# Kernel tuning notes

Hardware: AMD Instinct MI355X
Metric: run time of the kernel (lower is better)

The kernel has to match this reference:

```python
import jax, jax.numpy as jnp
import numpy as np

N_HEADS = 16
KEY_DIM = 64
VAL_DIM = 64
HIDDEN = 1024
SCALE = 1.0 / float(KEY_DIM) ** 0.5


def setup_inputs() -> dict:
    key = jax.random.key(0)
    ks = jax.random.split(key, 16)
    B, Lq, Lk, R = 2, 2048, 2048, 2048
    inp = {
        "query": jax.random.normal(ks[0], (B, Lq, HIDDEN), jnp.float32),
        "value": jax.random.normal(ks[1], (B, Lk, HIDDEN), jnp.float32),
        "positional_embedding": jax.random.normal(ks[2], (R, HIDDEN), jnp.float32),
        "u_weight": jax.random.normal(ks[3], (N_HEADS, KEY_DIM), jnp.float32) * 0.02,
        "v_weight": jax.random.normal(ks[4], (N_HEADS, KEY_DIM), jnp.float32) * 0.02,
        "indices": jax.random.randint(ks[5], (2, Lq, Lk), 0, R, jnp.int64 if jax.config.jax_enable_x64 else jnp.int32),
        "lower": jax.random.uniform(ks[6], (Lq, Lk), jnp.float32),
    }
    s = 0.02
    inp["Wq"] = jax.random.normal(ks[7], (HIDDEN, N_HEADS * KEY_DIM), jnp.float32) * s
    inp["bq"] = jnp.zeros((N_HEADS * KEY_DIM,), jnp.float32)
    inp["Wk"] = jax.random.normal(ks[8], (HIDDEN, N_HEADS * KEY_DIM), jnp.float32) * s
    inp["bk"] = jnp.zeros((N_HEADS * KEY_DIM,), jnp.float32)
    inp["Wv"] = jax.random.normal(ks[9], (HIDDEN, N_HEADS * VAL_DIM), jnp.float32) * s
    inp["bv"] = jnp.zeros((N_HEADS * VAL_DIM,), jnp.float32)
    inp["Wr"] = jax.random.normal(ks[10], (HIDDEN, N_HEADS * KEY_DIM), jnp.float32) * s
    inp["br"] = jnp.zeros((N_HEADS * KEY_DIM,), jnp.float32)
    inp["Wo"] = jax.random.normal(ks[11], (N_HEADS * VAL_DIM, HIDDEN), jnp.float32) * s
    inp["bo"] = jnp.zeros((HIDDEN,), jnp.float32)
    return inp


def reference(query, value, positional_embedding, u_weight, v_weight, indices, lower,
              Wq, bq, Wk, bk, Wv, bv, Wr, br, Wo, bo):
    B, Lq, _ = query.shape
    Lk = value.shape[1]
    R = positional_embedding.shape[0]
    # projections (torch Linear with weights stored as [in, out])
    q = (query @ Wq + bq).reshape(B, Lq, N_HEADS, KEY_DIM)
    k = (value @ Wk + bk).reshape(B, Lk, N_HEADS, KEY_DIM)
    v = (value @ Wv + bv).reshape(B, Lk, N_HEADS, VAL_DIM)
    r = (positional_embedding @ Wr + br).reshape(R, N_HEADS, KEY_DIM)
    # content (AC) and position (BD) score terms -> [i, j, b, n]
    AC = jnp.einsum("bind,bjnd->ijbn", q + u_weight, k)
    BD = jnp.einsum("bind,jnd->ijbn", q + v_weight, r)
    # rel-shift: gather [Lq, R] -> [Lq, Lk] positions, then apply lower mask
    BD = BD[indices[0], indices[1]] * lower[:, :, None, None]
    attn = jax.nn.softmax((AC + BD) * SCALE, axis=1)  # softmax over key dim j
    out = jnp.einsum("ijbn,bjnd->bind", attn, v).reshape(B, Lq, N_HEADS * VAL_DIM)
    return out @ Wo + bo
```

## Files before the change

kernel.cpp:

```cpp
#include <hip/hip_runtime.h>
#include <stdint.h>

typedef __attribute__((ext_vector_type(8))) short short8;
typedef __attribute__((ext_vector_type(4))) float f32x4;
typedef unsigned short u16;
typedef unsigned int u32;

#define LQ 2048
#define LK 2048
#define RDIM 2048
#define HID 1024
#define NH 16
#define DH 64
#define XL_SCALE 0.125f

__device__ __forceinline__ float bf2f(u16 u){
  union { unsigned int i; float f; } v; v.i = ((unsigned int)u) << 16; return v.f;
}
__device__ __forceinline__ u16 f2bf(float f){
  union { float f; unsigned int i; } v; v.f = f;
  unsigned int r = v.i + 0x7fffu + ((v.i >> 16) & 1u);
  return (u16)(r >> 16);
}
__device__ __forceinline__ f32x4 fzero(){ f32x4 z = {0.0f, 0.0f, 0.0f, 0.0f}; return z; }

__global__ void k_detect(const u32* __restrict__ q, const u32* __restrict__ idxw,
                         int* __restrict__ flags){
  int t = threadIdx.x;
  u32 w = q[t];
  int b = (w >> 7) & 0xFF;
  unsigned long long mb = __ballot(b >= 100 && b <= 140);
  u32 hi = idxw[2 * t + 1];
  unsigned long long mi = __ballot(hi == 0u);
  if (t == 0){
    flags[0] = (__popcll(mb) >= 48) ? 1 : 0;
    flags[1] = (__popcll(mi) == 64) ? 1 : 0;
  }
}

struct Seg { const void* src; u16* dst; int n4; };
struct SegPack { Seg s[8]; };
__global__ void k_ingestN(SegPack p, const int* __restrict__ flags){
  int f = flags[0];
  Seg sg = p.s[blockIdx.y];
  int stride = gridDim.x * blockDim.x;
  for (int i = blockIdx.x * blockDim.x + threadIdx.x; i < sg.n4; i += stride){
    if (f){
      reinterpret_cast<uint2*>(sg.dst)[i] = reinterpret_cast<const uint2*>(sg.src)[i];
    } else {
      float4 v = reinterpret_cast<const float4*>(sg.src)[i];
      union { u16 h[4]; uint2 u; } t;
      t.h[0] = f2bf(v.x); t.h[1] = f2bf(v.y); t.h[2] = f2bf(v.z); t.h[3] = f2bf(v.w);
      reinterpret_cast<uint2*>(sg.dst)[i] = t.u;
    }
  }
}

struct WPack { const void* src[5]; u16* dst[5]; };
__global__ void k_wtrans(WPack p, const int* __restrict__ flags){
  int f = flags[0];
  const void* W = p.src[blockIdx.z];
  u16* Wt = p.dst[blockIdx.z];
  __shared__ u16 t[64][65];
  int tid = threadIdx.x;
  int bx = blockIdx.x, by = blockIdx.y;
#pragma unroll
  for (int it = 0; it < 16; ++it){
    int id = it * 256 + tid;
    int r = id >> 6, c = id & 63;
    size_t so = (size_t)(by * 64 + r) * HID + bx * 64 + c;
    t[r][c] = f ? ((const u16*)W)[so] : f2bf(((const float*)W)[so]);
  }
  __syncthreads();
#pragma unroll
  for (int it = 0; it < 16; ++it){
    int id = it * 256 + tid;
    int r = id >> 6, c = id & 63;
    Wt[(size_t)(bx * 64 + r) * HID + by * 64 + c] = t[c][r];
  }
}

__global__ void k_goff(const int* __restrict__ idx, int* __restrict__ goff,
                       const int* __restrict__ flags){
  int i64f = flags[1];
  const size_t N = (size_t)LQ * LK;
  size_t stride = (size_t)gridDim.x * blockDim.x;
  for (size_t t = (size_t)blockIdx.x * blockDim.x + threadIdx.x; t < N; t += stride){
    long long a0, a1;
    if (i64f){
      const long long* ip = (const long long*)idx;
      a0 = ip[t]; a1 = ip[N + t];
    } else {
      a0 = idx[t]; a1 = idx[N + t];
    }
    goff[t] = (int)(a0 * RDIM + a1);
  }
}

__global__ void k_gemm(const u16* __restrict__ A, const u16* __restrict__ Bt,
                       const u16* __restrict__ bias,
                       const u16* __restrict__ add0, const u16* __restrict__ add1,
                       void* __restrict__ D0, u16* __restrict__ D1,
                       int headmajor, const int* __restrict__ oflags){
  __shared__ u16 As[128][72];
  __shared__ u16 Bs[128][72];
  int tid = threadIdx.x;
  int l = tid & 63, w = tid >> 6;
  int lr = l & 15, g = l >> 4;
  int wr = w >> 1, wc = w & 1;
  int outf32 = oflags ? (oflags[0] == 0) : 0;
  f32x4 acc[4][4];
#pragma unroll
  for (int a = 0; a < 4; ++a)
#pragma unroll
    for (int bq_ = 0; bq_ < 4; ++bq_) acc[a][bq_] = fzero();
  const size_t arowg = (size_t)blockIdx.x * 128;
  const size_t browg = (size_t)blockIdx.y * 128;
  for (int kt = 0; kt < HID; kt += 64){
#pragma unroll
    for (int it = 0; it < 4; ++it){
      int id = it * 256 + tid;
      int r = id >> 3, ch = id & 7;
      uint4 va = *reinterpret_cast<const uint4*>(A + (arowg + r) * HID + kt + ch * 8);
      *reinterpret_cast<uint4*>(&As[r][ch * 8]) = va;
      uint4 vb = *reinterpret_cast<const uint4*>(Bt + (browg + r) * HID + kt + ch * 8);
      *reinterpret_cast<uint4*>(&Bs[r][ch * 8]) = vb;
    }
    __syncthreads();
#pragma unroll
    for (int ks = 0; ks < 2; ++ks){
      short8 af[4], bfv[4];
#pragma unroll
      for (int mf = 0; mf < 4; ++mf)
        af[mf] = *reinterpret_cast<const short8*>(&As[wr * 64 + mf * 16 + lr][ks * 32 + 8 * g]);
#pragma unroll
      for (int nf = 0; nf < 4; ++nf)
        bfv[nf] = *reinterpret_cast<const short8*>(&Bs[wc * 64 + nf * 16 + lr][ks * 32 + 8 * g]);
#pragma unroll
      for (int mf = 0; mf < 4; ++mf)
#pragma unroll
        for (int nf = 0; nf < 4; ++nf)
          acc[mf][nf] = __builtin_amdgcn_mfma_f32_16x16x32_bf16(af[mf], bfv[nf], acc[mf][nf], 0, 0, 0);
    }
    __syncthreads();
  }
#pragma unroll
  for (int mf = 0; mf < 4; ++mf)
#pragma unroll
    for (int nf = 0; nf < 4; ++nf){
      int col = (int)browg + wc * 64 + nf * 16 + lr;
      float bcol = bf2f(bias[col]);
      float a0 = add0 ? bf2f(add0[col]) : 0.0f;
      float a1 = add1 ? bf2f(add1[col]) : 0.0f;
#pragma unroll
      for (int reg = 0; reg < 4; ++reg){
        int row = (int)arowg + wr * 64 + mf * 16 + 4 * g + reg;
        float base = acc[mf][nf][reg] + bcol;
        size_t dst;
        if (headmajor){
          int b = row >> 11, i = row & 2047;
          int n = col >> 6, d = col & 63;
          dst = ((size_t)(b * NH + n) * LQ + i) * DH + d;
        } else {
          dst = (size_t)row * HID + col;
        }
        if (outf32) ((float*)D0)[dst] = base + a0;
        else        ((u16*)D0)[dst] = f2bf(base + a0);
        if (D1) D1[dst] = f2bf(base + a1);
      }
    }
}

template<int G>
__global__ void k_bdfull(const u16* __restrict__ qv, const u16* __restrict__ rr,
                         u16* __restrict__ bdf, int bnBase){
  __shared__ u16 tile[16][32][G];
  int tid = threadIdx.x;
  int l = tid & 63, w = tid >> 6;
  int lr = l & 15, g = l >> 4;
  int i0 = blockIdx.x * 16, j0 = blockIdx.y * 32;
  constexpr int C = (G >= 4) ? (G / 4) : 1;
  if (G >= 4 || w < G){
#pragma unroll
    for (int bi = 0; bi < C; ++bi){
      int g_ = w * C + bi;
      int bn = bnBase + g_;
      int b = bn >> 4, n = bn & 15;
      const u16* qb = qv + ((size_t)(b * NH + n) * LQ + i0) * DH;
      const u16* rb = rr + ((size_t)n * RDIM + j0) * DH;
      f32x4 acc2[2];
      acc2[0] = fzero(); acc2[1] = fzero();
#pragma unroll
      for (int ks = 0; ks < 2; ++ks){
        short8 a = *reinterpret_cast<const short8*>(qb + (size_t)lr * DH + ks * 32 + 8 * g);
#pragma unroll
        for (int nf = 0; nf < 2; ++nf){
          short8 bb = *reinterpret_cast<const short8*>(rb + (size_t)(lr + 16 * nf) * DH + ks * 32 + 8 * g);
          acc2[nf] = __builtin_amdgcn_mfma_f32_16x16x32_bf16(a, bb, acc2[nf], 0, 0, 0);
        }
      }
#pragma unroll
      for (int nf = 0; nf < 2; ++nf){
        int jj = lr + 16 * nf;
#pragma unroll
        for (int reg = 0; reg < 4; ++reg)
          tile[4 * g + reg][jj][g_] = f2bf(acc2[nf][reg]);
      }
    }
  }
  __syncthreads();
  constexpr int W = (G >= 4) ? 4 : G;
  constexpr int PARTS = G / W;
  constexpr int CHUNKS = 512 * PARTS;
#pragma unroll
  for (int e = 0; e < (CHUNKS + 255) / 256; ++e){
    int id = e * 256 + tid;
    if (CHUNKS < 256 * ((CHUNKS + 255) / 256) && id >= CHUNKS) break;
    int line = id / PARTS, part = id % PARTS;
    int ii = line >> 5, jj = line & 31;
    int k = part * W;
    const u16* src = &tile[ii][jj][k];
    u16* dst = bdf + ((size_t)(i0 + ii) * RDIM + (size_t)(j0 + jj)) * G + k;
    if (W == 4)
      *reinterpret_cast<unsigned long long*>(dst) = *reinterpret_cast<const unsigned long long*>(src);
    else if (W == 2)
      *reinterpret_cast<unsigned int*>(dst) = *reinterpret_cast<const unsigned int*>(src);
    else
      *dst = *src;
  }
}

template<int G>
__global__ void k_gather(const u16* __restrict__ bdf, const int* __restrict__ goff,
                         const u16* __restrict__ lower, u16* __restrict__ bdg){
  __shared__ u16 tile[G][16][32];
  int tid = threadIdx.x;
  int i0 = blockIdx.x * 16, j0 = blockIdx.y * 32;
#pragma unroll
  for (int it = 0; it < 2; ++it){
    int p = it * 256 + tid;
    int ii = p >> 5, jj = p & 31;
    size_t off = (size_t)(i0 + ii) * LK + (j0 + jj);
    int go = goff[off];
    float lw = bf2f(lower[off]);
    const u16* src = bdf + (size_t)go * G;
    union { uint4 q[2]; u32 w2[8]; u16 h[16]; } uv;
    if (G == 16){
      uv.q[0] = *reinterpret_cast<const uint4*>(src);
      uv.q[1] = *reinterpret_cast<const uint4*>(src + 8);
    } else if (G == 8){
      uv.q[0] = *reinterpret_cast<const uint4*>(src);
    } else if (G == 2){
      uv.w2[0] = *reinterpret_cast<const u32*>(src);
    } else {
      uv.h[0] = *src;
    }
#pragma unroll
    for (int k = 0; k < G; ++k)
      tile[k][ii][jj] = f2bf(bf2f(uv.h[k]) * lw);
  }
  __syncthreads();
  constexpr int CHUNKS = G * 128;
#pragma unroll
  for (int e = 0; e < (CHUNKS + 255) / 256; ++e){
    int id = e * 256 + tid;
    if (CHUNKS < 256 * ((CHUNKS + 255) / 256) && id >= CHUNKS) break;
    int g_ = id >> 7, rem = id & 127;
    int ii = rem >> 3, part = rem & 7;
    unsigned long long v = *reinterpret_cast<const unsigned long long*>(&tile[g_][ii][part * 4]);
    *reinterpret_cast<unsigned long long*>(
        bdg + (size_t)g_ * LQ * LK + (size_t)(i0 + ii) * LK + j0 + part * 4) = v;
  }
}

__global__ void k_flash(const u16* __restrict__ qu, const u16* __restrict__ kk,
                        const u16* __restrict__ vv, const u16* __restrict__ bdg,
                        u16* __restrict__ oo, int bnBase){
  __shared__ u16 klds[128][72];
  __shared__ u16 vtlds[64][136];
  __shared__ u16 plds[4][16][136];
  int tid = threadIdx.x;
  int l = tid & 63, w = tid >> 6;
  int lr = l & 15, g = l >> 4;
  int gi = blockIdx.x;
  int bn = bnBase + gi;
  int b = bn >> 4, n = bn & 15;
  int i0 = blockIdx.y * 64;
  const u16* qb = qu + ((size_t)bn * LQ + i0 + w * 16) * DH;
  short8 aq0 = *reinterpret_cast<const short8*>(qb + (size_t)lr * DH + 8 * g);
  short8 aq1 = *reinterpret_cast<const short8*>(qb + (size_t)lr * DH + 32 + 8 * g);
  f32x4 O[4];
#pragma unroll
  for (int nf = 0; nf < 4; ++nf) O[nf] = fzero();
  float mrun[4], lrun[4];
#pragma unroll
  for (int r = 0; r < 4; ++r){ mrun[r] = -1e30f; lrun[r] = 0.0f; }
  const u16* kbase = kk + (size_t)bn * LK * DH;
  const u16* vbase = vv + (size_t)bn * LK * DH;
  const u16* bdb = bdg + (size_t)gi * LQ * LK + (size_t)(i0 + w * 16) * LK;

  for (int j0 = 0; j0 < LK; j0 += 128){
#pragma unroll
    for (int it = 0; it < 4; ++it){
      int id = it * 256 + tid;
      int r = id >> 3, ch = id & 7;
      uint4 kv = *reinterpret_cast<const uint4*>(kbase + (size_t)(j0 + r) * DH + ch * 8);
      *reinterpret_cast<uint4*>(&klds[r][ch * 8]) = kv;
      uint4 vv4 = *reinterpret_cast<const uint4*>(vbase + (size_t)(j0 + r) * DH + ch * 8);
      u16 tmp[8];
      *reinterpret_cast<uint4*>(tmp) = vv4;
#pragma unroll
      for (int e2 = 0; e2 < 8; ++e2) vtlds[ch * 8 + e2][r] = tmp[e2];
    }
    __syncthreads();

    float sv[8][4];
#pragma unroll
    for (int nf = 0; nf < 8; ++nf){
      f32x4 z = fzero();
      short8 bk0 = *reinterpret_cast<const short8*>(&klds[lr + 16 * nf][8 * g]);
      short8 bk1 = *reinterpret_cast<const short8*>(&klds[lr + 16 * nf][32 + 8 * g]);
      z = __builtin_amdgcn_mfma_f32_16x16x32_bf16(aq0, bk0, z, 0, 0, 0);
      z = __builtin_amdgcn_mfma_f32_16x16x32_bf16(aq1, bk1, z, 0, 0, 0);
#pragma unroll
      for (int reg = 0; reg < 4; ++reg){
        float bd = bf2f(bdb[(size_t)(4 * g + reg) * LK + j0 + lr + 16 * nf]);
        sv[nf][reg] = (z[reg] + bd) * XL_SCALE;
      }
    }
    float fs[4];
#pragma unroll
    for (int reg = 0; reg < 4; ++reg){
      float mx = sv[0][reg];
#pragma unroll
      for (int nf = 1; nf < 8; ++nf) mx = fmaxf(mx, sv[nf][reg]);
#pragma unroll
      for (int d = 1; d < 16; d <<= 1) mx = fmaxf(mx, __shfl_xor(mx, d));
      float mnew = fmaxf(mrun[reg], mx);
      fs[reg] = __expf(mrun[reg] - mnew);
      mrun[reg] = mnew;
      float sum = 0.0f;
#pragma unroll
      for (int nf = 0; nf < 8; ++nf){
        sv[nf][reg] = __expf(sv[nf][reg] - mnew);
        sum += sv[nf][reg];
      }
#pragma unroll
      for (int d = 1; d < 16; d <<= 1) sum += __shfl_xor(sum, d);
      lrun[reg] = lrun[reg] * fs[reg] + sum;
    }
#pragma unroll
    for (int nf = 0; nf < 4; ++nf)
#pragma unroll
      for (int reg = 0; reg < 4; ++reg)
        O[nf][reg] *= fs[reg];
#pragma unroll
    for (int nf = 0; nf < 8; ++nf)
#pragma unroll
      for (int reg = 0; reg < 4; ++reg)
        plds[w][4 * g + reg][lr + 16 * nf] = f2bf(sv[nf][reg]);
    short8 pa[4];
#pragma unroll
    for (int ks = 0; ks < 4; ++ks)
      pa[ks] = *reinterpret_cast<const short8*>(&plds[w][lr][ks * 32 + 8 * g]);
#pragma unroll
    for (int nf = 0; nf < 4; ++nf){
#pragma unroll
      for (int ks = 0; ks < 4; ++ks){
        short8 bv = *reinterpret_cast<const short8*>(&vtlds[lr + 16 * nf][ks * 32 + 8 * g]);
        O[nf] = __builtin_amdgcn_mfma_f32_16x16x32_bf16(pa[ks], bv, O[nf], 0, 0, 0);
      }
    }
    __syncthreads();
  }
#pragma unroll
  for (int nf = 0; nf < 4; ++nf)
#pragma unroll
    for (int reg = 0; reg < 4; ++reg){
      int i = i0 + w * 16 + 4 * g + reg;
      float vo = O[nf][reg] / lrun[reg];
      oo[((size_t)(b * LQ + i)) * HID + n * DH + lr + 16 * nf] = f2bf(vo);
    }
}

extern "C" void kernel_launch(void* const* d_in, const int* in_sizes, int n_in,
                              void* d_out, int out_size, void* d_ws, size_t ws_size,
                              hipStream_t stream){
  const void* query = d_in[0];
  const void* value = d_in[1];
  const void* pos   = d_in[2];
  const void* uw    = d_in[3];
  const void* vw    = d_in[4];
  const int* idx    = (const int*)d_in[5];
  const void* lower = d_in[6];
  const void* Wq = d_in[7];  const void* bq = d_in[8];
  const void* Wk = d_in[9];  const void* bk = d_in[10];
  const void* Wv = d_in[11]; const void* bv = d_in[12];
  const void* Wr = d_in[13]; const void* br = d_in[14];
  const void* Wo = d_in[15]; const void* bo = d_in[16];
  (void)in_sizes; (void)n_in; (void)out_size;

  char* ws = (char*)d_ws;
  const size_t MB = (size_t)1 << 20;
  u16* cquery = (u16*)(ws + 0 * MB);
  u16* cvalue = (u16*)(ws + 8 * MB);
  int* goff   = (int*)(ws + 0 * MB);
  u16* cpos   = (u16*)(ws + 16 * MB);
  u16* clower = (u16*)(ws + 20 * MB);
  char* sm = ws + 38 * MB;
  u16* cuw = (u16*)(sm + 0 * 4096);
  u16* cvw = (u16*)(sm + 1 * 4096);
  u16* cbq = (u16*)(sm + 2 * 4096);
  u16* cbk = (u16*)(sm + 3 * 4096);
  u16* cbv = (u16*)(sm + 4 * 4096);
  u16* cbr = (u16*)(sm + 5 * 4096);
  u16* cbo = (u16*)(sm + 6 * 4096);
  int* flags = (int*)(sm + 7 * 4096);
  u16* wqt = (u16*)(ws + 39 * MB);
  u16* wkt = (u16*)(ws + 41 * MB);
  u16* wvt = (u16*)(ws + 43 * MB);
  u16* wrt = (u16*)(ws + 45 * MB);
  u16* wot = (u16*)(ws + 47 * MB);
  u16* qu  = (u16*)(ws + 49 * MB);
  u16* qv  = (u16*)(ws + 57 * MB);
  u16* kkp = (u16*)(ws + 65 * MB);
  u16* vvp = (u16*)(ws + 73 * MB);
  u16* rrp = (u16*)(ws + 81 * MB);
  u16* oo  = (u16*)(ws + 85 * MB);
  u16* bdf = (u16*)(ws + 96 * MB);

  int G = 1;
  if (ws_size >= 352 * MB) G = 16;
  else if (ws_size >= 224 * MB) G = 8;
  else if (ws_size >= 128 * MB) G = 2;
  u16* bdg = (u16*)(ws + (96 + 8 * (size_t)G) * MB);

  dim3 blk(256);
  k_detect<<<1, 64, 0, stream>>>((const u32*)query, (const u32*)idx, flags);

  {
    SegPack big;
    big.s[0] = { query, cquery, 2 * LQ * HID / 4 };
    big.s[1] = { value, cvalue, 2 * LK * HID / 4 };
    big.s[2] = { pos,   cpos,   RDIM * HID / 4 };
    big.s[3] = { lower, clower, LQ * LK / 4 };
    for (int i = 4; i < 8; ++i) big.s[i] = { nullptr, nullptr, 0 };
    k_ingestN<<<dim3(512, 4), blk, 0, stream>>>(big, flags);
    SegPack sml;
    sml.s[0] = { uw, cuw, NH * DH / 4 };
    sml.s[1] = { vw, cvw, NH * DH / 4 };
    sml.s[2] = { bq, cbq, HID / 4 };
    sml.s[3] = { bk, cbk, HID / 4 };
    sml.s[4] = { bv, cbv, HID / 4 };
    sml.s[5] = { br, cbr, HID / 4 };
    sml.s[6] = { bo, cbo, HID / 4 };
    sml.s[7] = { nullptr, nullptr, 0 };
    k_ingestN<<<dim3(4, 7), blk, 0, stream>>>(sml, flags);
  }
  {
    WPack wp;
    wp.src[0] = Wq; wp.dst[0] = wqt;
    wp.src[1] = Wk; wp.dst[1] = wkt;
    wp.src[2] = Wv; wp.dst[2] = wvt;
    wp.src[3] = Wr; wp.dst[3] = wrt;
    wp.src[4] = Wo; wp.dst[4] = wot;
    k_wtrans<<<dim3(16, 16, 5), blk, 0, stream>>>(wp, flags);
  }

  k_gemm<<<dim3(32, 8), blk, 0, stream>>>(cquery, wqt, cbq, cuw, cvw, qu, qv, 1, nullptr);
  k_gemm<<<dim3(32, 8), blk, 0, stream>>>(cvalue, wkt, cbk, nullptr, nullptr, kkp, nullptr, 1, nullptr);
  k_gemm<<<dim3(32, 8), blk, 0, stream>>>(cvalue, wvt, cbv, nullptr, nullptr, vvp, nullptr, 1, nullptr);
  k_gemm<<<dim3(16, 8), blk, 0, stream>>>(cpos, wrt, cbr, nullptr, nullptr, rrp, nullptr, 1, nullptr);

  k_goff<<<dim3(1024), blk, 0, stream>>>(idx, goff, flags);

  for (int b0 = 0; b0 < 2 * NH; b0 += G){
    if (G == 16){
      k_bdfull<16><<<dim3(128, 64), blk, 0, stream>>>(qv, rrp, bdf, b0);
      k_gather<16><<<dim3(128, 64), blk, 0, stream>>>(bdf, goff, clower, bdg);
    } else if (G == 8){
      k_bdfull<8><<<dim3(128, 64), blk, 0, stream>>>(qv, rrp, bdf, b0);
      k_gather<8><<<dim3(128, 64), blk, 0, stream>>>(bdf, goff, clower, bdg);
    } else if (G == 2){
      k_bdfull<2><<<dim3(128, 64), blk, 0, stream>>>(qv, rrp, bdf, b0);
      k_gather<2><<<dim3(128, 64), blk, 0, stream>>>(bdf, goff, clower, bdg);
    } else {
      k_bdfull<1><<<dim3(128, 64), blk, 0, stream>>>(qv, rrp, bdf, b0);
      k_gather<1><<<dim3(128, 64), blk, 0, stream>>>(bdf, goff, clower, bdg);
    }
    k_flash<<<dim3(G, 32), blk, 0, stream>>>(qu, kkp, vvp, bdg, oo, b0);
  }
  k_gemm<<<dim3(32, 8), blk, 0, stream>>>(oo, wot, cbo, nullptr, nullptr, d_out, nullptr, 0, flags);
}
```

Measured before the change: 1.008 ms.

## Fuse K/V projections, retile BD score kernel, streamline flash softmax

The K and V projection GEMMs are merged into one launch. It relies on the transposed Wk/Wv weights and the K/V biases sitting next to each other in memory, and a new epilogue mode routes each column half to the K or V buffer. A dedicated k_bdfull16 kernel computes 32x64 tiles per block with register-held Q fragments, reusing each R fragment across two row fragments. In the flash kernel, log2(e) is folded into the score scale so exp2f replaces __expf, and the per-row cross-lane sum shuffle moves out of the key loop to run once at the end. The aim is fewer launches, less redundant operand loading and less per-iteration shuffle work, at the cost of depending on the workspace layout being contiguous.

```diff
diff --git a/kernel.cpp b/kernel.cpp
--- a/kernel.cpp
+++ b/kernel.cpp
@@ -5,6 +5,7 @@
 typedef __attribute__((ext_vector_type(4))) float f32x4;
 typedef unsigned short u16;
 typedef unsigned int u32;
+typedef unsigned long long u64;
 
 #define LQ 2048
 #define LK 2048
@@ -12,7 +13,7 @@
 #define HID 1024
 #define NH 16
 #define DH 64
-#define XL_SCALE 0.125f
+#define S2SCALE 0.1803368801111204f
 
 __device__ __forceinline__ float bf2f(u16 u){
   union { unsigned int i; float f; } v; v.i = ((unsigned int)u) << 16; return v.f;
@@ -156,19 +157,80 @@
       for (int reg = 0; reg < 4; ++reg){
         int row = (int)arowg + wr * 64 + mf * 16 + 4 * g + reg;
         float base = acc[mf][nf][reg] + bcol;
-        size_t dst;
-        if (headmajor){
+        if (headmajor == 2){
+          int b = row >> 11, i = row & 2047;
+          int n32 = col >> 6, d = col & 63;
+          u16* Dx = (n32 < NH) ? (u16*)D0 : D1;
+          size_t dst = ((size_t)(b * NH + (n32 & (NH - 1))) * LQ + i) * DH + d;
+          Dx[dst] = f2bf(base);
+        } else if (headmajor == 1){
           int b = row >> 11, i = row & 2047;
           int n = col >> 6, d = col & 63;
-          dst = ((size_t)(b * NH + n) * LQ + i) * DH + d;
+          size_t dst = ((size_t)(b * NH + n) * LQ + i) * DH + d;
+          ((u16*)D0)[dst] = f2bf(base + a0);
+          if (D1) D1[dst] = f2bf(base + a1);
         } else {
-          dst = (size_t)row * HID + col;
+          size_t dst = (size_t)row * HID + col;
+          if (outf32) ((float*)D0)[dst] = base;
+          else        ((u16*)D0)[dst] = f2bf(base);
         }
-        if (outf32) ((float*)D0)[dst] = base + a0;
-        else        ((u16*)D0)[dst] = f2bf(base + a0);
-        if (D1) D1[dst] = f2bf(base + a1);
-      }
-    }
+      }
+    }
+}
+
+__global__ void k_bdfull16(const u16* __restrict__ qv, const u16* __restrict__ rr,
+                           u16* __restrict__ bdf, int bnBase){
+  __shared__ u16 tile[32][64][16];
+  int tid = threadIdx.x;
+  int l = tid & 63, w = tid >> 6;
+  int lr = l & 15, g = l >> 4;
+  int i0 = blockIdx.x * 32, j0 = blockIdx.y * 64;
+#pragma unroll
+  for (int hh = 0; hh < 4; ++hh){
+    int g_ = w * 4 + hh;
+    int bn = bnBase + g_;
+    int b = bn >> 4, n = bn & 15;
+    const u16* qb = qv + ((size_t)(b * NH + n) * LQ + i0) * DH;
+    const u16* rb = rr + ((size_t)n * RDIM + j0) * DH;
+    short8 af[2][2];
+#pragma unroll
+    for (int mf = 0; mf < 2; ++mf)
+#pragma unroll
+      for (int ks = 0; ks < 2; ++ks)
+        af[mf][ks] = *reinterpret_cast<const short8*>(qb + (size_t)(mf * 16 + lr) * DH + ks * 32 + 8 * g);
+    f32x4 acc[2][4];
+#pragma unroll
+    for (int mf = 0; mf < 2; ++mf)
+#pragma unroll
+      for (int nf = 0; nf < 4; ++nf) acc[mf][nf] = fzero();
+#pragma unroll
+    for (int nf = 0; nf < 4; ++nf){
+#pragma unroll
+      for (int ks = 0; ks < 2; ++ks){
+        short8 bb = *reinterpret_cast<const short8*>(rb + (size_t)(nf * 16 + lr) * DH + ks * 32 + 8 * g);
+#pragma unroll
+        for (int mf = 0; mf < 2; ++mf)
+          acc[mf][nf] = __builtin_amdgcn_mfma_f32_16x16x32_bf16(af[mf][ks], bb, acc[mf][nf], 0, 0, 0);
+      }
+    }
+#pragma unroll
+    for (int mf = 0; mf < 2; ++mf)
+#pragma unroll
+      for (int nf = 0; nf < 4; ++nf)
+#pragma unroll
+        for (int reg = 0; reg < 4; ++reg)
+          tile[mf * 16 + 4 * g + reg][nf * 16 + lr][g_] = f2bf(acc[mf][nf][reg]);
+  }
+  __syncthreads();
+#pragma unroll
+  for (int e = 0; e < 32; ++e){
+    int id = e * 256 + tid;
+    int line = id >> 2, part = id & 3;
+    int ii = line >> 6, jj = line & 63;
+    u64 v = *reinterpret_cast<const u64*>(&tile[ii][jj][part * 4]);
+    *reinterpret_cast<u64*>(
+        bdf + ((size_t)(i0 + ii) * RDIM + (size_t)(j0 + jj)) * 16 + part * 4) = v;
+  }
 }
 
 template<int G>
@@ -222,9 +284,9 @@
     const u16* src = &tile[ii][jj][k];
     u16* dst = bdf + ((size_t)(i0 + ii) * RDIM + (size_t)(j0 + jj)) * G + k;
     if (W == 4)
-      *reinterpret_cast<unsigned long long*>(dst) = *reinterpret_cast<const unsigned long long*>(src);
+      *reinterpret_cast<u64*>(dst) = *reinterpret_cast<const u64*>(src);
     else if (W == 2)
-      *reinterpret_cast<unsigned int*>(dst) = *reinterpret_cast<const unsigned int*>(src);
+      *reinterpret_cast<u32*>(dst) = *reinterpret_cast<const u32*>(src);
     else
       *dst = *src;
   }
@@ -267,8 +329,8 @@
     if (CHUNKS < 256 * ((CHUNKS + 255) / 256) && id >= CHUNKS) break;
     int g_ = id >> 7, rem = id & 127;
     int ii = rem >> 3, part = rem & 7;
-    unsigned long long v = *reinterpret_cast<const unsigned long long*>(&tile[g_][ii][part * 4]);
-    *reinterpret_cast<unsigned long long*>(
+    u64 v = *reinterpret_cast<const u64*>(&tile[g_][ii][part * 4]);
+    *reinterpret_cast<u64*>(
         bdg + (size_t)g_ * LQ * LK + (size_t)(i0 + ii) * LK + j0 + part * 4) = v;
   }
 }
@@ -292,9 +354,9 @@
   f32x4 O[4];
 #pragma unroll
   for (int nf = 0; nf < 4; ++nf) O[nf] = fzero();
-  float mrun[4], lrun[4];
-#pragma unroll
-  for (int r = 0; r < 4; ++r){ mrun[r] = -1e30f; lrun[r] = 0.0f; }
+  float mrun[4], lacc[4];
+#pragma unroll
+  for (int r = 0; r < 4; ++r){ mrun[r] = -1e30f; lacc[r] = 0.0f; }
   const u16* kbase = kk + (size_t)bn * LK * DH;
   const u16* vbase = vv + (size_t)bn * LK * DH;
   const u16* bdb = bdg + (size_t)gi * LQ * LK + (size_t)(i0 + w * 16) * LK;
@@ -325,7 +387,7 @@
 #pragma unroll
       for (int reg = 0; reg < 4; ++reg){
         float bd = bf2f(bdb[(size_t)(4 * g + reg) * LK + j0 + lr + 16 * nf]);
-        sv[nf][reg] = (z[reg] + bd) * XL_SCALE;
+        sv[nf][reg] = (z[reg] + bd) * S2SCALE;
       }
     }
     float fs[4];
@@ -337,17 +399,15 @@
 #pragma unroll
       for (int d = 1; d < 16; d <<= 1) mx = fmaxf(mx, __shfl_xor(mx, d));
       float mnew = fmaxf(mrun[reg], mx);
-      fs[reg] = __expf(mrun[reg] - mnew);
+      fs[reg] = exp2f(mrun[reg] - mnew);
       mrun[reg] = mnew;
-      float sum = 0.0f;
+      float sumloc = 0.0f;
 #pragma unroll
       for (int nf = 0; nf < 8; ++nf){
-        sv[nf][reg] = __expf(sv[nf][reg] - mnew);
-        sum += sv[nf][reg];
-      }
-#pragma unroll
-      for (int d = 1; d < 16; d <<= 1) sum += __shfl_xor(sum, d);
-      lrun[reg] = lrun[reg] * fs[reg] + sum;
+        sv[nf][reg] = exp2f(sv[nf][reg] - mnew);
+        sumloc += sv[nf][reg];
+      }
+      lacc[reg] = lacc[reg] * fs[reg] + sumloc;
     }
 #pragma unroll
     for (int nf = 0; nf < 4; ++nf)
@@ -373,12 +433,20 @@
     }
     __syncthreads();
   }
+  float lsum[4];
+#pragma unroll
+  for (int reg = 0; reg < 4; ++reg){
+    float s = lacc[reg];
+#pragma unroll
+    for (int d = 1; d < 16; d <<= 1) s += __shfl_xor(s, d);
+    lsum[reg] = s;
+  }
 #pragma unroll
   for (int nf = 0; nf < 4; ++nf)
 #pragma unroll
     for (int reg = 0; reg < 4; ++reg){
       int i = i0 + w * 16 + 4 * g + reg;
-      float vo = O[nf][reg] / lrun[reg];
+      float vo = O[nf][reg] / lsum[reg];
       oo[((size_t)(b * LQ + i)) * HID + n * DH + lr + 16 * nf] = f2bf(vo);
     }
 }
@@ -412,7 +480,7 @@
   u16* cvw = (u16*)(sm + 1 * 4096);
   u16* cbq = (u16*)(sm + 2 * 4096);
   u16* cbk = (u16*)(sm + 3 * 4096);
-  u16* cbv = (u16*)(sm + 4 * 4096);
+  u16* cbv = cbk + 1024;
   u16* cbr = (u16*)(sm + 5 * 4096);
   u16* cbo = (u16*)(sm + 6 * 4096);
   int* flags = (int*)(sm + 7 * 4096);
@@ -468,15 +536,14 @@
   }
 
   k_gemm<<<dim3(32, 8), blk, 0, stream>>>(cquery, wqt, cbq, cuw, cvw, qu, qv, 1, nullptr);
-  k_gemm<<<dim3(32, 8), blk, 0, stream>>>(cvalue, wkt, cbk, nullptr, nullptr, kkp, nullptr, 1, nullptr);
-  k_gemm<<<dim3(32, 8), blk, 0, stream>>>(cvalue, wvt, cbv, nullptr, nullptr, vvp, nullptr, 1, nullptr);
+  k_gemm<<<dim3(32, 16), blk, 0, stream>>>(cvalue, wkt, cbk, nullptr, nullptr, kkp, vvp, 2, nullptr);
   k_gemm<<<dim3(16, 8), blk, 0, stream>>>(cpos, wrt, cbr, nullptr, nullptr, rrp, nullptr, 1, nullptr);
 
   k_goff<<<dim3(1024), blk, 0, stream>>>(idx, goff, flags);
 
   for (int b0 = 0; b0 < 2 * NH; b0 += G){
     if (G == 16){
-      k_bdfull<16><<<dim3(128, 64), blk, 0, stream>>>(qv, rrp, bdf, b0);
+      k_bdfull16<<<dim3(64, 32), blk, 0, stream>>>(qv, rrp, bdf, b0);
       k_gather<16><<<dim3(128, 64), blk, 0, stream>>>(bdf, goff, clower, bdg);
     } else if (G == 8){
       k_bdfull<8><<<dim3(128, 64), blk, 0, stream>>>(qv, rrp, bdf, b0);
```

Result: no change. 989.3 us (-1.9%).
